# Kernel tuning notes

Hardware: AMD Instinct MI355X
Metric: run time of the kernel (lower is better)

The kernel has to match this reference:

```python
import jax, jax.numpy as jnp
import numpy as np

N_NODES = 100000
N_EDGES = 1600000


def _norms(src, dst, n_nodes, dtype):
    # DGL GraphConv norm='both': scale src by out-degree^{-1/2}, dst by in-degree^{-1/2}
    ones = jnp.ones((src.shape[0],), dtype=dtype)
    deg_out = jax.ops.segment_sum(ones, src, num_segments=n_nodes)
    deg_in = jax.ops.segment_sum(ones, dst, num_segments=n_nodes)
    inv_sqrt_out = jnp.where(deg_out > 0, jax.lax.rsqrt(jnp.maximum(deg_out, 1.0)), 0.0)
    inv_sqrt_in = jnp.where(deg_in > 0, jax.lax.rsqrt(jnp.maximum(deg_in, 1.0)), 0.0)
    return inv_sqrt_out, inv_sqrt_in


def _graph_conv(x, W, src, dst, inv_sqrt_out, inv_sqrt_in, n_nodes, relu):
    # norm='both': out = D_in^{-1/2} A D_out^{-1/2} x W
    h = x * inv_sqrt_out[:, None]
    h = h @ W                      # dense transform before aggregation
    msg = h[src]                   # gather messages along edges [E, F]
    agg = jax.ops.segment_sum(msg, dst, num_segments=n_nodes)
    out = agg * inv_sqrt_in[:, None]
    return jax.nn.relu(out) if relu else out


def setup_inputs() -> dict:
    key = jax.random.key(0)
    k1, k2, k3, k4, k5, k6 = jax.random.split(key, 6)
    in_dim, h_dim, out_dim = 128, 128, 64
    features = jax.random.normal(k1, (N_NODES, in_dim), dtype=jnp.float32)
    W1 = jax.random.normal(k2, (in_dim, h_dim), dtype=jnp.float32) * (1.0 / np.sqrt(in_dim))
    W2 = jax.random.normal(k3, (h_dim, h_dim), dtype=jnp.float32) * (1.0 / np.sqrt(h_dim))
    W3 = jax.random.normal(k4, (h_dim, out_dim), dtype=jnp.float32) * (1.0 / np.sqrt(h_dim))
    src = jax.random.randint(k5, (N_EDGES,), 0, N_NODES, dtype=jnp.int32)
    dst = jax.random.randint(k6, (N_EDGES,), 0, N_NODES, dtype=jnp.int32)
    return {"features": features, "W1": W1, "W2": W2, "W3": W3, "src": src, "dst": dst}


def reference(features, W1, W2, W3, src, dst):
    inv_sqrt_out, inv_sqrt_in = _norms(src, dst, N_NODES, features.dtype)
    h = _graph_conv(features, W1, src, dst, inv_sqrt_out, inv_sqrt_in, N_NODES, relu=True)
    h = _graph_conv(h, W2, src, dst, inv_sqrt_out, inv_sqrt_in, N_NODES, relu=True)
    h = _graph_conv(h, W3, src, dst, inv_sqrt_out, inv_sqrt_in, N_NODES, relu=False)
    return h
```

## Files before the change

kernel.cpp:

```cpp
#include <hip/hip_runtime.h>


typedef float f32x4 __attribute__((ext_vector_type(4)));
typedef __bf16 bf16x8 __attribute__((ext_vector_type(8)));

constexpr int CAP = 5120;
constexpr int MAXNB = 400;

__device__ inline unsigned short f2bf_bits(float f) {
    unsigned u = __float_as_uint(f);
    unsigned r = u + 0x7fff + ((u >> 16) & 1);
    return (unsigned short)(r >> 16);
}
__device__ inline float bf_bits2f(unsigned short s) {
    return __uint_as_float(((unsigned)s) << 16);
}
__device__ inline float bf_lo(unsigned v) { return __uint_as_float(v << 16); }
__device__ inline float bf_hi(unsigned v) { return __uint_as_float(v & 0xffff0000u); }


__global__ __launch_bounds__(512) void bucket_scatter(
    const int* __restrict__ src, const int* __restrict__ dst,
    int* __restrict__ cur_d, int* __restrict__ cur_s,
    int* __restrict__ bpair, int* __restrict__ bsrc, int E, int NB) {
    __shared__ int hd[MAXNB], hs[MAXNB], bd[MAXNB], bs[MAXNB];
    const int tid = threadIdx.x;
    for (int i = tid; i < NB; i += 512) { hd[i] = 0; hs[i] = 0; }
    __syncthreads();

    const int base = (blockIdx.x * 512 + tid) * 8;
    int s[8], d[8], rd[8], rs[8];
    bool va[8];
    if (base + 8 <= E) {
        const int4 s0 = *(const int4*)(src + base);
        const int4 s1 = *(const int4*)(src + base + 4);
        const int4 d0 = *(const int4*)(dst + base);
        const int4 d1 = *(const int4*)(dst + base + 4);
        s[0] = s0.x; s[1] = s0.y; s[2] = s0.z; s[3] = s0.w;
        s[4] = s1.x; s[5] = s1.y; s[6] = s1.z; s[7] = s1.w;
        d[0] = d0.x; d[1] = d0.y; d[2] = d0.z; d[3] = d0.w;
        d[4] = d1.x; d[5] = d1.y; d[6] = d1.z; d[7] = d1.w;
#pragma unroll
        for (int j = 0; j < 8; ++j) va[j] = true;
    } else {
#pragma unroll
        for (int j = 0; j < 8; ++j) {
            const int e = base + j;
            va[j] = e < E;
            const int ec = va[j] ? e : 0;
            s[j] = src[ec];
            d[j] = dst[ec];
        }
    }
#pragma unroll
    for (int j = 0; j < 8; ++j) {
        if (va[j]) {
            rd[j] = atomicAdd(&hd[d[j] >> 8], 1);
            rs[j] = atomicAdd(&hs[s[j] >> 8], 1);
        }
    }
    __syncthreads();
    for (int i = tid; i < NB; i += 512) {
        bd[i] = hd[i] ? atomicAdd(&cur_d[i], hd[i]) : 0;
        bs[i] = hs[i] ? atomicAdd(&cur_s[i], hs[i]) : 0;
    }
    __syncthreads();
#pragma unroll
    for (int j = 0; j < 8; ++j) {
        if (va[j]) {
            const int b = d[j] >> 8;
            const int pos = bd[b] + rd[j];
            if (pos < CAP) bpair[(size_t)b * CAP + pos] = (s[j] << 8) | (d[j] & 255);
            const int c = s[j] >> 8;
            const int ps = bs[c] + rs[j];
            if (ps < CAP) bsrc[(size_t)c * CAP + ps] = s[j];
        }
    }
}

__global__ __launch_bounds__(512) void bucket_scan(
    const int* __restrict__ cur_d, int* __restrict__ bbase, int NB) {
    __shared__ int s[512];
    const int tid = threadIdx.x;
    s[tid] = (tid < NB) ? cur_d[tid] : 0;
    __syncthreads();
    for (int off = 1; off < 512; off <<= 1) {
        int v = (tid >= off) ? s[tid - off] : 0;
        __syncthreads();
        s[tid] += v;
        __syncthreads();
    }
    if (tid < NB) bbase[tid] = (tid > 0) ? s[tid - 1] : 0;
}

__global__ __launch_bounds__(256) void csr_outdeg(
    const int* __restrict__ bpair, const int* __restrict__ bsrc,
    const int* __restrict__ bcnt_d, const int* __restrict__ bcnt_s,
    const int* __restrict__ bbase, int* __restrict__ row_ptr,
    int* __restrict__ col, float* __restrict__ isi, float* __restrict__ iso,
    float* __restrict__ fscale, int N, int NB) {
    __shared__ int h[256], hs[256], sc[256], cur[256];
    const int b = blockIdx.x;
    const int tid = threadIdx.x;
    const int cnt = min(bcnt_d[b], CAP);
    const int scnt = min(bcnt_s[b], CAP);
    const int base = bbase[b];
    const int* pairs = bpair + (size_t)b * CAP;
    const int* svals = bsrc + (size_t)b * CAP;
    h[tid] = 0;
    hs[tid] = 0;
    __syncthreads();
    for (int i = tid; i < cnt; i += 256) atomicAdd(&h[pairs[i] & 255], 1);
    for (int i = tid; i < scnt; i += 256) atomicAdd(&hs[svals[i] & 255], 1);
    __syncthreads();
    sc[tid] = h[tid];
    __syncthreads();
    for (int off = 1; off < 256; off <<= 1) {
        int v = (tid >= off) ? sc[tid - off] : 0;
        __syncthreads();
        sc[tid] += v;
        __syncthreads();
    }
    const int lp = sc[tid] - h[tid];
    const int node = b * 256 + tid;
    if (node < N) {
        row_ptr[node] = base + lp;
        const float di = (h[tid] > 0) ? rsqrtf((float)h[tid]) : 0.f;
        const float dw = (hs[tid] > 0) ? rsqrtf((float)hs[tid]) : 0.f;
        isi[node] = di;
        iso[node] = dw;
        fscale[node] = di * dw;
    }
    if (b == NB - 1 && tid == 0) row_ptr[N] = base + cnt;
    cur[tid] = lp;
    __syncthreads();
    for (int i = tid; i < cnt; i += 256) {
        const int p = pairs[i];
        const int pos = base + atomicAdd(&cur[p & 255], 1);
        col[pos] = p >> 8;
    }
}


__device__ inline void wpack1(const float* W, unsigned short* Wh,
                              unsigned short* Wl, int t, int F) {
    const int n = t >> 7, k = t & 127;
    const float w = W[k * F + n];
    const unsigned short hb = f2bf_bits(w);
    Wh[t] = hb;
    Wl[t] = f2bf_bits(w - bf_bits2f(hb));
}

__global__ __launch_bounds__(256) void wpack_all(
    const float* __restrict__ W1, const float* __restrict__ W2,
    const float* __restrict__ W3, unsigned short* __restrict__ Wt1h,
    unsigned short* __restrict__ Wt1l, unsigned short* __restrict__ Wt2h,
    unsigned short* __restrict__ Wt2l, unsigned short* __restrict__ Wt3h,
    unsigned short* __restrict__ Wt3l) {
    int t = blockIdx.x * 256 + threadIdx.x;
    if (t < 16384) {
        wpack1(W1, Wt1h, Wt1l, t, 128);
    } else if (t < 32768) {
        wpack1(W2, Wt2h, Wt2l, t - 16384, 128);
    } else if (t < 40960) {
        wpack1(W3, Wt3h, Wt3l, t - 32768, 64);
    }
}


template <int F>
__global__ __launch_bounds__(256) void gemm_mfma(
    const float* __restrict__ X, const unsigned short* __restrict__ Wt_hi,
    const unsigned short* __restrict__ Wt_lo, const float* __restrict__ so,
    unsigned short* __restrict__ Y, int N) {
    constexpr int NT = F / 16;
    const int wave = threadIdx.x >> 6;
    const int lane = threadIdx.x & 63;
    const int r0 = blockIdx.x * 128 + wave * 32;
    const int l15 = lane & 15;
    const int quad = lane >> 4;

    const int rowA0 = min(r0 + l15, N - 1);
    const int rowA1 = min(r0 + 16 + l15, N - 1);
    const float s0 = so[rowA0];
    const float s1 = so[rowA1];
    const float* pX0 = X + (size_t)rowA0 * 128 + quad * 8;
    const float* pX1 = X + (size_t)rowA1 * 128 + quad * 8;

    f32x4 acc0[NT], acc1[NT];
    const f32x4 z = {0.f, 0.f, 0.f, 0.f};
#pragma unroll
    for (int t = 0; t < NT; ++t) { acc0[t] = z; acc1[t] = z; }

    union AB { bf16x8 v; unsigned short u[8]; };

#pragma unroll
    for (int s = 0; s < 4; ++s) {
        const int kb = s * 32;
        AB bh[NT], bl[NT];
#pragma unroll
        for (int t = 0; t < NT; ++t) {
            const int n = t * 16 + l15;
            bh[t].v = *(const bf16x8*)(Wt_hi + n * 128 + kb + quad * 8);
            bl[t].v = *(const bf16x8*)(Wt_lo + n * 128 + kb + quad * 8);
        }
        float a[8];
        *(f32x4*)&a[0] = *(const f32x4*)(pX0 + kb);
        *(f32x4*)&a[4] = *(const f32x4*)(pX0 + kb + 4);
        AB ah, al;
#pragma unroll
        for (int j = 0; j < 8; ++j) {
            float x = a[j] * s0;
            unsigned short hb = f2bf_bits(x);
            ah.u[j] = hb;
            al.u[j] = f2bf_bits(x - bf_bits2f(hb));
        }
#pragma unroll
        for (int t = 0; t < NT; ++t) {
            acc0[t] = __builtin_amdgcn_mfma_f32_16x16x32_bf16(ah.v, bh[t].v, acc0[t], 0, 0, 0);
            acc0[t] = __builtin_amdgcn_mfma_f32_16x16x32_bf16(al.v, bh[t].v, acc0[t], 0, 0, 0);
            acc0[t] = __builtin_amdgcn_mfma_f32_16x16x32_bf16(ah.v, bl[t].v, acc0[t], 0, 0, 0);
        }
        *(f32x4*)&a[0] = *(const f32x4*)(pX1 + kb);
        *(f32x4*)&a[4] = *(const f32x4*)(pX1 + kb + 4);
#pragma unroll
        for (int j = 0; j < 8; ++j) {
            float x = a[j] * s1;
            unsigned short hb = f2bf_bits(x);
            ah.u[j] = hb;
            al.u[j] = f2bf_bits(x - bf_bits2f(hb));
        }
#pragma unroll
        for (int t = 0; t < NT; ++t) {
            acc1[t] = __builtin_amdgcn_mfma_f32_16x16x32_bf16(ah.v, bh[t].v, acc1[t], 0, 0, 0);
            acc1[t] = __builtin_amdgcn_mfma_f32_16x16x32_bf16(al.v, bh[t].v, acc1[t], 0, 0, 0);
            acc1[t] = __builtin_amdgcn_mfma_f32_16x16x32_bf16(ah.v, bl[t].v, acc1[t], 0, 0, 0);
        }
    }

#pragma unroll
    for (int t = 0; t < NT; ++t) {
#pragma unroll
        for (int r = 0; r < 4; ++r) {
            int node0 = r0 + quad * 4 + r;
            if (node0 < N) Y[(size_t)node0 * F + t * 16 + l15] = f2bf_bits(acc0[t][r]);
            int node1 = r0 + 16 + quad * 4 + r;
            if (node1 < N) Y[(size_t)node1 * F + t * 16 + l15] = f2bf_bits(acc1[t][r]);
        }
    }
}


template <int F>
__global__ __launch_bounds__(256) void gemm_bf16A(
    const unsigned short* __restrict__ A, const unsigned short* __restrict__ Wt_hi,
    const unsigned short* __restrict__ Wt_lo, unsigned short* __restrict__ Y, int N) {
    constexpr int NT = F / 16;
    const int wave = threadIdx.x >> 6;
    const int lane = threadIdx.x & 63;
    const int r0 = blockIdx.x * 128 + wave * 32;
    const int l15 = lane & 15;
    const int quad = lane >> 4;

    const int rowA0 = min(r0 + l15, N - 1);
    const int rowA1 = min(r0 + 16 + l15, N - 1);
    const unsigned short* pA0 = A + (size_t)rowA0 * 128 + quad * 8;
    const unsigned short* pA1 = A + (size_t)rowA1 * 128 + quad * 8;

    f32x4 acc0[NT], acc1[NT];
    const f32x4 z = {0.f, 0.f, 0.f, 0.f};
#pragma unroll
    for (int t = 0; t < NT; ++t) { acc0[t] = z; acc1[t] = z; }

#pragma unroll
    for (int s = 0; s < 4; ++s) {
        const int kb = s * 32;
        bf16x8 bh[NT], bl[NT];
#pragma unroll
        for (int t = 0; t < NT; ++t) {
            const int n = t * 16 + l15;
            bh[t] = *(const bf16x8*)(Wt_hi + n * 128 + kb + quad * 8);
            bl[t] = *(const bf16x8*)(Wt_lo + n * 128 + kb + quad * 8);
        }
        const bf16x8 a0 = *(const bf16x8*)(pA0 + kb);
        const bf16x8 a1 = *(const bf16x8*)(pA1 + kb);
#pragma unroll
        for (int t = 0; t < NT; ++t) {
            acc0[t] = __builtin_amdgcn_mfma_f32_16x16x32_bf16(a0, bh[t], acc0[t], 0, 0, 0);
            acc0[t] = __builtin_amdgcn_mfma_f32_16x16x32_bf16(a0, bl[t], acc0[t], 0, 0, 0);
            acc1[t] = __builtin_amdgcn_mfma_f32_16x16x32_bf16(a1, bh[t], acc1[t], 0, 0, 0);
            acc1[t] = __builtin_amdgcn_mfma_f32_16x16x32_bf16(a1, bl[t], acc1[t], 0, 0, 0);
        }
    }

#pragma unroll
    for (int t = 0; t < NT; ++t) {
#pragma unroll
        for (int r = 0; r < 4; ++r) {
            int node0 = r0 + quad * 4 + r;
            if (node0 < N) Y[(size_t)node0 * F + t * 16 + l15] = f2bf_bits(acc0[t][r]);
            int node1 = r0 + 16 + quad * 4 + r;
            if (node1 < N) Y[(size_t)node1 * F + t * 16 + l15] = f2bf_bits(acc1[t][r]);
        }
    }
}


__global__ __launch_bounds__(256) void gather128_bf16(
    const unsigned short* __restrict__ msg, const int* __restrict__ row_ptr,
    const int* __restrict__ col, const float* __restrict__ fscale,
    unsigned short* __restrict__ outA, int N) {
    const int wave = (blockIdx.x * 256 + threadIdx.x) >> 6;
    const int lane = threadIdx.x & 63;
    if (wave >= N) return;
    const int start = row_ptr[wave], end = row_ptr[wave + 1];
    const unsigned* m32 = (const unsigned*)msg;

    float a0 = 0.f, a1 = 0.f, b0 = 0.f, b1 = 0.f;
    int e = start;
    const int efull = start + ((end - start) & ~7);
    for (; e < efull; e += 8) {
        int c[8];
#pragma unroll
        for (int j = 0; j < 8; ++j) c[j] = col[e + j];
        unsigned v[8];
#pragma unroll
        for (int j = 0; j < 8; ++j) v[j] = m32[(size_t)c[j] * 64 + lane];
#pragma unroll
        for (int j = 0; j < 8; j += 2) {
            a0 += bf_lo(v[j]);     a1 += bf_hi(v[j]);
            b0 += bf_lo(v[j + 1]); b1 += bf_hi(v[j + 1]);
        }
    }
    const int rem = end - e;
    if (rem > 0) {
        int c[8];
#pragma unroll
        for (int j = 0; j < 8; ++j) c[j] = col[e + min(j, rem - 1)];
        unsigned v[8];
#pragma unroll
        for (int j = 0; j < 8; ++j) v[j] = m32[(size_t)c[j] * 64 + lane];
#pragma unroll
        for (int j = 0; j < 8; ++j) {
            a0 += (j < rem) ? bf_lo(v[j]) : 0.f;
            a1 += (j < rem) ? bf_hi(v[j]) : 0.f;
        }
    }
    const float sc = fscale[wave];
    a0 = fmaxf((a0 + b0) * sc, 0.f);
    a1 = fmaxf((a1 + b1) * sc, 0.f);
    const unsigned packed =
        ((unsigned)f2bf_bits(a1) << 16) | (unsigned)f2bf_bits(a0);
    ((unsigned*)outA)[(size_t)wave * 64 + lane] = packed;
}

__global__ __launch_bounds__(256) void gather64(
    const unsigned short* __restrict__ msg, const int* __restrict__ row_ptr,
    const int* __restrict__ col, const float* __restrict__ isi,
    float* __restrict__ out, int N) {
    const int w = (blockIdx.x * 256 + threadIdx.x) >> 6;
    const int lane = threadIdx.x & 63;
    const int node = w * 2 + (lane >> 5);
    const int j31 = lane & 31;
    if (node >= N) return;
    const int start = row_ptr[node], end = row_ptr[node + 1];
    const unsigned* m32 = (const unsigned*)msg;

    float a0 = 0.f, a1 = 0.f, b0 = 0.f, b1 = 0.f;
    int e = start;
    const int efull = start + ((end - start) & ~7);
    for (; e < efull; e += 8) {
        int c[8];
#pragma unroll
        for (int j = 0; j < 8; ++j) c[j] = col[e + j];
        unsigned v[8];
#pragma unroll
        for (int j = 0; j < 8; ++j) v[j] = m32[(size_t)c[j] * 32 + j31];
#pragma unroll
        for (int j = 0; j < 8; j += 2) {
            a0 += bf_lo(v[j]);     a1 += bf_hi(v[j]);
            b0 += bf_lo(v[j + 1]); b1 += bf_hi(v[j + 1]);
        }
    }
    const int rem = end - e;
    if (rem > 0) {
        int c[8];
#pragma unroll
        for (int j = 0; j < 8; ++j) c[j] = col[e + min(j, rem - 1)];
        unsigned v[8];
#pragma unroll
        for (int j = 0; j < 8; ++j) v[j] = m32[(size_t)c[j] * 32 + j31];
#pragma unroll
        for (int j = 0; j < 8; ++j) {
            a0 += (j < rem) ? bf_lo(v[j]) : 0.f;
            a1 += (j < rem) ? bf_hi(v[j]) : 0.f;
        }
    }
    const float sc = isi[node];
    *(float2*)(out + (size_t)node * 64 + j31 * 2) =
        make_float2((a0 + b0) * sc, (a1 + b1) * sc);
}


extern "C" void kernel_launch(void* const* d_in, const int* in_sizes, int n_in,
                              void* d_out, int out_size, void* d_ws, size_t ws_size,
                              hipStream_t stream) {
    const float* features = (const float*)d_in[0];
    const float* W1 = (const float*)d_in[1];
    const float* W2 = (const float*)d_in[2];
    const float* W3 = (const float*)d_in[3];
    const int* src = (const int*)d_in[4];
    const int* dst = (const int*)d_in[5];
    float* out = (float*)d_out;

    const int N = in_sizes[0] / 128;
    const int E = in_sizes[4];
    const int NB = (N + 255) >> 8;

    char* ws = (char*)d_ws;
    unsigned short* A = (unsigned short*)ws;      ws += (size_t)N * 128 * 2;
    unsigned short* Y = (unsigned short*)ws;      ws += (size_t)N * 128 * 2;
    int* row_ptr = (int*)ws;                      ws += (size_t)(N + 1) * 4;
    int* col = (int*)ws;                          ws += (size_t)E * 4;
    float* iso = (float*)ws;                      ws += (size_t)N * 4;
    float* isi = (float*)ws;                      ws += (size_t)N * 4;
    float* fscale = (float*)ws;                   ws += (size_t)N * 4;
    int* cur_d = (int*)ws;                        ws += MAXNB * 4;
    int* cur_s = (int*)ws;                        ws += MAXNB * 4;
    int* bbase = (int*)ws;                        ws += MAXNB * 4;
    unsigned short* Wt1h = (unsigned short*)ws;   ws += 128 * 128 * 2;
    unsigned short* Wt1l = (unsigned short*)ws;   ws += 128 * 128 * 2;
    unsigned short* Wt2h = (unsigned short*)ws;   ws += 128 * 128 * 2;
    unsigned short* Wt2l = (unsigned short*)ws;   ws += 128 * 128 * 2;
    unsigned short* Wt3h = (unsigned short*)ws;   ws += 64 * 128 * 2;
    unsigned short* Wt3l = (unsigned short*)ws;   ws += 64 * 128 * 2;

    int* bpair = (int*)A;
    int* bsrc = (int*)((char*)A + (size_t)MAXNB * CAP * 4);

    wpack_all<<<160, 256, 0, stream>>>(W1, W2, W3, Wt1h, Wt1l, Wt2h, Wt2l, Wt3h, Wt3l);
    hipMemsetAsync(cur_d, 0, 2 * MAXNB * sizeof(int), stream);
    const int gBS = (E + 4095) / 4096;
    bucket_scatter<<<gBS, 512, 0, stream>>>(src, dst, cur_d, cur_s, bpair, bsrc, E, NB);
    bucket_scan<<<1, 512, 0, stream>>>(cur_d, bbase, NB);
    csr_outdeg<<<NB, 256, 0, stream>>>(bpair, bsrc, cur_d, cur_s, bbase, row_ptr,
                                       col, isi, iso, fscale, N, NB);

    const int gG = (N + 127) / 128;
    const int ga128 = (N * 64 + 255) / 256;
    const int ga64 = ((N / 2 + 1) * 64 + 255) / 256;

    gemm_mfma<128><<<gG, 256, 0, stream>>>(features, Wt1h, Wt1l, iso, Y, N);
    gather128_bf16<<<ga128, 256, 0, stream>>>(Y, row_ptr, col, fscale, A, N);
    gemm_bf16A<128><<<gG, 256, 0, stream>>>(A, Wt2h, Wt2l, Y, N);
    gather128_bf16<<<ga128, 256, 0, stream>>>(Y, row_ptr, col, fscale, A, N);
    gemm_bf16A<64><<<gG, 256, 0, stream>>>(A, Wt3h, Wt3l, Y, N);
    gather64<<<ga64, 256, 0, stream>>>(Y, row_ptr, col, isi, out, N);
}
```

Measured before the change: 414.0 us.

## Permute GEMM output layout for vectorized stores and 8-byte gather loads

The GEMM epilogues now pack each lane's bf16 outputs across tiles into one contiguous 16- or 8-byte vector store, so message rows are stored in a permuted feature order. To compensate, W2 and W3 are packed with a matching permutation of their K dimension, so the next layer consumes the permuted activations directly. The gather kernels switch to 8-byte loads, with each half-wave handling alternate edges and a cross-lane shuffle reduction at the end. The final gather un-permutes when writing the fp32 output. The aim is fewer, wider memory transactions in both the GEMM stores and the edge gathers, at the cost of shuffle reductions and idle lanes during writeback.

```diff
diff --git a/kernel.cpp b/kernel.cpp
--- a/kernel.cpp
+++ b/kernel.cpp
@@ -17,6 +17,9 @@
 }
 __device__ inline float bf_lo(unsigned v) { return __uint_as_float(v << 16); }
 __device__ inline float bf_hi(unsigned v) { return __uint_as_float(v & 0xffff0000u); }
+__device__ inline unsigned pack_bf2(float x0, float x1) {
+    return ((unsigned)f2bf_bits(x1) << 16) | (unsigned)f2bf_bits(x0);
+}
 
 
 __global__ __launch_bounds__(512) void bucket_scatter(
@@ -142,9 +145,19 @@
 }
 
 
-__device__ inline void wpack1(const float* W, unsigned short* Wh,
-                              unsigned short* Wl, int t, int F) {
+__device__ inline void wpack_true(const float* W, unsigned short* Wh,
+                                  unsigned short* Wl, int t, int F) {
     const int n = t >> 7, k = t & 127;
+    const float w = W[k * F + n];
+    const unsigned short hb = f2bf_bits(w);
+    Wh[t] = hb;
+    Wl[t] = f2bf_bits(w - bf_bits2f(hb));
+}
+
+__device__ inline void wpack_perm(const float* W, unsigned short* Wh,
+                                  unsigned short* Wl, int t, int F) {
+    const int n = t >> 7, phi = t & 127;
+    const int k = ((phi & 7) << 4) | (phi >> 3);
     const float w = W[k * F + n];
     const unsigned short hb = f2bf_bits(w);
     Wh[t] = hb;
@@ -159,11 +172,27 @@
     unsigned short* __restrict__ Wt3l) {
     int t = blockIdx.x * 256 + threadIdx.x;
     if (t < 16384) {
-        wpack1(W1, Wt1h, Wt1l, t, 128);
+        wpack_true(W1, Wt1h, Wt1l, t, 128);
     } else if (t < 32768) {
-        wpack1(W2, Wt2h, Wt2l, t - 16384, 128);
+        wpack_perm(W2, Wt2h, Wt2l, t - 16384, 128);
     } else if (t < 40960) {
-        wpack1(W3, Wt3h, Wt3l, t - 32768, 64);
+        wpack_perm(W3, Wt3h, Wt3l, t - 32768, 64);
+    }
+}
+
+
+template <int NT>
+__device__ inline void store_row_perm(unsigned short* __restrict__ Y,
+                                      const f32x4* acc, int r, size_t node,
+                                      int l15) {
+    unsigned pk[NT / 2];
+#pragma unroll
+    for (int t = 0; t < NT; t += 2) pk[t / 2] = pack_bf2(acc[t][r], acc[t + 1][r]);
+    unsigned short* p = Y + node * (NT * 16) + l15 * NT;
+    if constexpr (NT == 8) {
+        *(uint4*)p = make_uint4(pk[0], pk[1], pk[2], pk[3]);
+    } else {
+        *(uint2*)p = make_uint2(pk[0], pk[1]);
     }
 }
 
@@ -239,14 +268,11 @@
     }
 
 #pragma unroll
-    for (int t = 0; t < NT; ++t) {
-#pragma unroll
-        for (int r = 0; r < 4; ++r) {
-            int node0 = r0 + quad * 4 + r;
-            if (node0 < N) Y[(size_t)node0 * F + t * 16 + l15] = f2bf_bits(acc0[t][r]);
-            int node1 = r0 + 16 + quad * 4 + r;
-            if (node1 < N) Y[(size_t)node1 * F + t * 16 + l15] = f2bf_bits(acc1[t][r]);
-        }
+    for (int r = 0; r < 4; ++r) {
+        const int node0 = r0 + quad * 4 + r;
+        if (node0 < N) store_row_perm<NT>(Y, acc0, r, (size_t)node0, l15);
+        const int node1 = r0 + 16 + quad * 4 + r;
+        if (node1 < N) store_row_perm<NT>(Y, acc1, r, (size_t)node1, l15);
     }
 }
 
@@ -294,14 +320,11 @@
     }
 
 #pragma unroll
-    for (int t = 0; t < NT; ++t) {
-#pragma unroll
-        for (int r = 0; r < 4; ++r) {
-            int node0 = r0 + quad * 4 + r;
-            if (node0 < N) Y[(size_t)node0 * F + t * 16 + l15] = f2bf_bits(acc0[t][r]);
-            int node1 = r0 + 16 + quad * 4 + r;
-            if (node1 < N) Y[(size_t)node1 * F + t * 16 + l15] = f2bf_bits(acc1[t][r]);
-        }
+    for (int r = 0; r < 4; ++r) {
+        const int node0 = r0 + quad * 4 + r;
+        if (node0 < N) store_row_perm<NT>(Y, acc0, r, (size_t)node0, l15);
+        const int node1 = r0 + 16 + quad * 4 + r;
+        if (node1 < N) store_row_perm<NT>(Y, acc1, r, (size_t)node1, l15);
     }
 }
 
@@ -313,45 +336,52 @@
     const int wave = (blockIdx.x * 256 + threadIdx.x) >> 6;
     const int lane = threadIdx.x & 63;
     if (wave >= N) return;
+    const int es = lane >> 5;
+    const int h = lane & 31;
     const int start = row_ptr[wave], end = row_ptr[wave + 1];
-    const unsigned* m32 = (const unsigned*)msg;
-
-    float a0 = 0.f, a1 = 0.f, b0 = 0.f, b1 = 0.f;
+    const uint2* m64 = (const uint2*)msg;
+
+    float a0 = 0.f, a1 = 0.f, a2 = 0.f, a3 = 0.f;
     int e = start;
     const int efull = start + ((end - start) & ~7);
     for (; e < efull; e += 8) {
-        int c[8];
-#pragma unroll
-        for (int j = 0; j < 8; ++j) c[j] = col[e + j];
-        unsigned v[8];
-#pragma unroll
-        for (int j = 0; j < 8; ++j) v[j] = m32[(size_t)c[j] * 64 + lane];
-#pragma unroll
-        for (int j = 0; j < 8; j += 2) {
-            a0 += bf_lo(v[j]);     a1 += bf_hi(v[j]);
-            b0 += bf_lo(v[j + 1]); b1 += bf_hi(v[j + 1]);
+        int c[4];
+        uint2 v[4];
+#pragma unroll
+        for (int jj = 0; jj < 4; ++jj) c[jj] = col[e + 2 * jj + es];
+#pragma unroll
+        for (int jj = 0; jj < 4; ++jj) v[jj] = m64[(size_t)c[jj] * 32 + h];
+#pragma unroll
+        for (int jj = 0; jj < 4; ++jj) {
+            a0 += bf_lo(v[jj].x); a1 += bf_hi(v[jj].x);
+            a2 += bf_lo(v[jj].y); a3 += bf_hi(v[jj].y);
         }
     }
     const int rem = end - e;
     if (rem > 0) {
-        int c[8];
-#pragma unroll
-        for (int j = 0; j < 8; ++j) c[j] = col[e + min(j, rem - 1)];
-        unsigned v[8];
-#pragma unroll
-        for (int j = 0; j < 8; ++j) v[j] = m32[(size_t)c[j] * 64 + lane];
-#pragma unroll
-        for (int j = 0; j < 8; ++j) {
-            a0 += (j < rem) ? bf_lo(v[j]) : 0.f;
-            a1 += (j < rem) ? bf_hi(v[j]) : 0.f;
-        }
-    }
-    const float sc = fscale[wave];
-    a0 = fmaxf((a0 + b0) * sc, 0.f);
-    a1 = fmaxf((a1 + b1) * sc, 0.f);
-    const unsigned packed =
-        ((unsigned)f2bf_bits(a1) << 16) | (unsigned)f2bf_bits(a0);
-    ((unsigned*)outA)[(size_t)wave * 64 + lane] = packed;
+        int c[4];
+        uint2 v[4];
+#pragma unroll
+        for (int jj = 0; jj < 4; ++jj) c[jj] = col[e + min(2 * jj + es, rem - 1)];
+#pragma unroll
+        for (int jj = 0; jj < 4; ++jj) v[jj] = m64[(size_t)c[jj] * 32 + h];
+#pragma unroll
+        for (int jj = 0; jj < 4; ++jj) {
+            if (2 * jj + es < rem) {
+                a0 += bf_lo(v[jj].x); a1 += bf_hi(v[jj].x);
+                a2 += bf_lo(v[jj].y); a3 += bf_hi(v[jj].y);
+            }
+        }
+    }
+    a0 += __shfl_xor(a0, 32); a1 += __shfl_xor(a1, 32);
+    a2 += __shfl_xor(a2, 32); a3 += __shfl_xor(a3, 32);
+    if (es == 0) {
+        const float sc = fscale[wave];
+        a0 = fmaxf(a0 * sc, 0.f); a1 = fmaxf(a1 * sc, 0.f);
+        a2 = fmaxf(a2 * sc, 0.f); a3 = fmaxf(a3 * sc, 0.f);
+        uint2 p = make_uint2(pack_bf2(a0, a1), pack_bf2(a2, a3));
+        *(uint2*)(outA + (size_t)wave * 128 + h * 4) = p;
+    }
 }
 
 __global__ __launch_bounds__(256) void gather64(
@@ -361,44 +391,54 @@
     const int w = (blockIdx.x * 256 + threadIdx.x) >> 6;
     const int lane = threadIdx.x & 63;
     const int node = w * 2 + (lane >> 5);
-    const int j31 = lane & 31;
     if (node >= N) return;
+    const int es = (lane >> 4) & 1;
+    const int h = lane & 15;
     const int start = row_ptr[node], end = row_ptr[node + 1];
-    const unsigned* m32 = (const unsigned*)msg;
-
-    float a0 = 0.f, a1 = 0.f, b0 = 0.f, b1 = 0.f;
+    const uint2* m64 = (const uint2*)msg;
+
+    float a0 = 0.f, a1 = 0.f, a2 = 0.f, a3 = 0.f;
     int e = start;
     const int efull = start + ((end - start) & ~7);
     for (; e < efull; e += 8) {
-        int c[8];
-#pragma unroll
-        for (int j = 0; j < 8; ++j) c[j] = col[e + j];
-        unsigned v[8];
-#pragma unroll
-        for (int j = 0; j < 8; ++j) v[j] = m32[(size_t)c[j] * 32 + j31];
-#pragma unroll
-        for (int j = 0; j < 8; j += 2) {
-            a0 += bf_lo(v[j]);     a1 += bf_hi(v[j]);
-            b0 += bf_lo(v[j + 1]); b1 += bf_hi(v[j + 1]);
+        int c[4];
+        uint2 v[4];
+#pragma unroll
+        for (int jj = 0; jj < 4; ++jj) c[jj] = col[e + 2 * jj + es];
+#pragma unroll
+        for (int jj = 0; jj < 4; ++jj) v[jj] = m64[(size_t)c[jj] * 16 + h];
+#pragma unroll
+        for (int jj = 0; jj < 4; ++jj) {
+            a0 += bf_lo(v[jj].x); a1 += bf_hi(v[jj].x);
+            a2 += bf_lo(v[jj].y); a3 += bf_hi(v[jj].y);
         }
     }
     const int rem = end - e;
     if (rem > 0) {
-        int c[8];
-#pragma unroll
-        for (int j = 0; j < 8; ++j) c[j] = col[e + min(j, rem - 1)];
-        unsigned v[8];
-#pragma unroll
-        for (int j = 0; j < 8; ++j) v[j] = m32[(size_t)c[j] * 32 + j31];
-#pragma unroll
-        for (int j = 0; j < 8; ++j) {
-            a0 += (j < rem) ? bf_lo(v[j]) : 0.f;
-            a1 += (j < rem) ? bf_hi(v[j]) : 0.f;
-        }
-    }
-    const float sc = isi[node];
-    *(float2*)(out + (size_t)node * 64 + j31 * 2) =
-        make_float2((a0 + b0) * sc, (a1 + b1) * sc);
+        int c[4];
+        uint2 v[4];
+#pragma unroll
+        for (int jj = 0; jj < 4; ++jj) c[jj] = col[e + min(2 * jj + es, rem - 1)];
+#pragma unroll
+        for (int jj = 0; jj < 4; ++jj) v[jj] = m64[(size_t)c[jj] * 16 + h];
+#pragma unroll
+        for (int jj = 0; jj < 4; ++jj) {
+            if (2 * jj + es < rem) {
+                a0 += bf_lo(v[jj].x); a1 += bf_hi(v[jj].x);
+                a2 += bf_lo(v[jj].y); a3 += bf_hi(v[jj].y);
+            }
+        }
+    }
+    a0 += __shfl_xor(a0, 16); a1 += __shfl_xor(a1, 16);
+    a2 += __shfl_xor(a2, 16); a3 += __shfl_xor(a3, 16);
+    if (es == 0) {
+        const float sc = isi[node];
+        float* ob = out + (size_t)node * 64;
+        ob[h] = a0 * sc;
+        ob[h + 16] = a1 * sc;
+        ob[h + 32] = a2 * sc;
+        ob[h + 48] = a3 * sc;
+    }
 }
 
 
```

Result: no change. 417.7 us (+0.9%).
